# Kernel optimization log

Hardware: AMD Instinct MI355X
Metric: run time of the kernel (lower is better)

Reference implementation:

```python
import jax, jax.numpy as jnp
import numpy as np

N_ENT = 50000
N_REL = 500
N_DIM = 256
K = 4            # num_blocks; n_arity = 3 -> arch has K**3 = 64 entries
B = 1024


def setup_inputs() -> dict:
    key = jax.random.key(0)
    k0, k1, k2, k3 = jax.random.split(key, 4)
    facts = jax.random.randint(k0, (B, 3), 0, N_REL)          # head, tail, rela (all < n_rel <= n_ent)
    arch = jax.random.randint(k1, (K ** 3,), 0, 3)            # selects op in {0, 1, -1}
    ent_w = jax.random.normal(k2, (N_ENT, N_DIM), dtype=jnp.float32) * 0.05  # xavier-ish scale
    rel_w = jax.random.normal(k3, (N_REL, N_DIM), dtype=jnp.float32) * 0.05
    return {
        "facts": facts,
        "arch": arch,
        "ent_w": ent_w,
        "rel_w": rel_w,
        "bne_gamma": jnp.ones((N_DIM,), jnp.float32),
        "bne_beta": jnp.zeros((N_DIM,), jnp.float32),
        "bnr_gamma": jnp.ones((N_DIM,), jnp.float32),
        "bnr_beta": jnp.zeros((N_DIM,), jnp.float32),
    }


def _bn(x, gamma, beta, eps=1e-5):
    # BatchNorm1d in training mode: biased batch statistics over the batch dim.
    m = jnp.mean(x, axis=0)
    v = jnp.var(x, axis=0)
    return (x - m) * jax.lax.rsqrt(v + eps) * gamma + beta


def _bce(p, y):
    # torch F.binary_cross_entropy clamps log terms at -100
    logp = jnp.maximum(jnp.log(p), -100.0)
    log1mp = jnp.maximum(jnp.log1p(-p), -100.0)
    return -jnp.mean(y * logp + (1.0 - y) * log1mp)


def reference(facts, arch, ent_w, rel_w, bne_gamma, bne_beta, bnr_gamma, bnr_beta):
    L = N_DIM // K
    h, t, r = facts[:, 0], facts[:, 1], facts[:, 2]
    # separate BN calls for head / tail batches, as in the torch code (dropout is eval-mode identity)
    he = _bn(ent_w[h], bne_gamma, bne_beta).reshape(-1, K, L)   # [B, K, L]
    te = _bn(ent_w[t], bne_gamma, bne_beta).reshape(-1, K, L)
    re = _bn(rel_w[r], bnr_gamma, bnr_beta).reshape(-1, K, L)
    # alpha[i,j,k] = ops[op_idx[i*K*K + j*K + k]] in {0, 1, -1}
    alpha = jnp.asarray([0.0, 1.0, -1.0], dtype=ent_w.dtype)[arch].reshape(K, K, K)
    # fused extend + inner_vec + inner_alpha_bi + sum-over-blocks:
    # last_idx=2 (head side, rela x tail): vec[b,k,l] = sum_{i,j} alpha[i,j,k] r[b,i,l] t[b,j,l]
    head_vec = jnp.einsum('ijk,bil,bjl->bkl', alpha, re, te).reshape(-1, N_DIM)
    # last_idx=1 (tail side, rela x head): vec[b,k,l] = sum_{i,j} alpha[i,k,j] r[b,i,l] h[b,j,l]
    tail_vec = jnp.einsum('ikj,bil,bjl->bkl', alpha, re, he).reshape(-1, N_DIM)
    head_p = jax.nn.softmax(head_vec @ ent_w.T, axis=1)         # [B, N_ENT]
    tail_p = jax.nn.softmax(tail_vec @ ent_w.T, axis=1)
    head_label = jax.nn.one_hot(h, N_ENT, dtype=head_p.dtype)
    tail_label = jax.nn.one_hot(t, N_ENT, dtype=tail_p.dtype)
    return _bce(head_p, head_label) + _bce(tail_p, tail_label)
```

## Files before the change

### kernel.cpp

```cpp
#include <hip/hip_runtime.h>

#define N_ENT   50000
#define N_ENT_P 50048
#define NDIM    256
#define BATCH   1024
#define MROWS   2048
#define BM      128
#define BN      128
#define BK      64
#define NTILES  391
#define NSTRIP  32
#define SHIFT   30.0f

typedef __attribute__((ext_vector_type(8))) short short8;
typedef __attribute__((ext_vector_type(4))) float f32x4;

__device__ __forceinline__ unsigned short f2bf(float f) {
  unsigned int u = __float_as_uint(f);
  u += 0x7fffu + ((u >> 16) & 1u);
  return (unsigned short)(u >> 16);
}

__device__ __forceinline__ void async16(const void* g, void* lds) {
  __builtin_amdgcn_global_load_lds(
      (const __attribute__((address_space(1))) unsigned int*)g,
      (__attribute__((address_space(3))) unsigned int*)lds,
      16, 0, 0);
}

__global__ void k_convert(const float* __restrict__ ent_w,
                          unsigned short* __restrict__ Wb) {
  int t = blockIdx.x * 256 + threadIdx.x;
  int row = t >> 6, c4 = (t & 63) << 2;
  ushort4 v;
  if (row < N_ENT) {
    float4 f = *(const float4*)(ent_w + row * NDIM + c4);
    v.x = f2bf(f.x); v.y = f2bf(f.y); v.z = f2bf(f.z); v.w = f2bf(f.w);
  } else {
    v.x = v.y = v.z = v.w = 0;
  }
  *(ushort4*)(Wb + row * NDIM + c4) = v;
}

__global__ void k_stats(const int* __restrict__ facts,
                        const float* __restrict__ ent_w,
                        const float* __restrict__ rel_w,
                        float* __restrict__ stats) {
  int seg = blockIdx.y;
  int d = threadIdx.x;
  const float* tab = (seg == 2) ? rel_w : ent_w;
  int r0 = blockIdx.x * 16;
  int idxs[16];
#pragma unroll
  for (int i = 0; i < 16; ++i) idxs[i] = facts[(r0 + i) * 3 + seg];
  float s = 0.f, s2 = 0.f;
#pragma unroll
  for (int i = 0; i < 16; ++i) {
    float v = tab[idxs[i] * NDIM + d];
    s += v; s2 += v * v;
  }
  atomicAdd(&stats[(seg * 2 + 0) * NDIM + d], s);
  atomicAdd(&stats[(seg * 2 + 1) * NDIM + d], s2);
}

__global__ void k_vectors(const int* __restrict__ facts, const int* __restrict__ arch,
                          const float* __restrict__ ent_w, const float* __restrict__ rel_w,
                          const float* __restrict__ bne_g, const float* __restrict__ bne_b,
                          const float* __restrict__ bnr_g, const float* __restrict__ bnr_b,
                          const float* __restrict__ stats,
                          unsigned short* __restrict__ HVb, float* __restrict__ zlab) {
  __shared__ float sh_he[256], sh_te[256], sh_re[256], sh_alpha[64], sh_red[16];
  int b = blockIdx.x, d = threadIdx.x;
  int h = facts[b * 3 + 0], t = facts[b * 3 + 1], r = facts[b * 3 + 2];
  const float inv = 1.0f / (float)BATCH;
  float mh = stats[0 * 256 + d] * inv, vh = stats[1 * 256 + d] * inv - mh * mh;
  float mt = stats[2 * 256 + d] * inv, vt = stats[3 * 256 + d] * inv - mt * mt;
  float mr = stats[4 * 256 + d] * inv, vr = stats[5 * 256 + d] * inv - mr * mr;
  float sch = rsqrtf(vh + 1e-5f) * bne_g[d], shh = bne_b[d] - mh * sch;
  float sct = rsqrtf(vt + 1e-5f) * bne_g[d], sht = bne_b[d] - mt * sct;
  float scr = rsqrtf(vr + 1e-5f) * bnr_g[d], shr = bnr_b[d] - mr * scr;
  sh_he[d] = ent_w[h * NDIM + d] * sch + shh;
  sh_te[d] = ent_w[t * NDIM + d] * sct + sht;
  sh_re[d] = rel_w[r * NDIM + d] * scr + shr;
  if (d < 64) {
    int a = arch[d];
    sh_alpha[d] = (a == 0) ? 0.f : ((a == 1) ? 1.f : -1.f);
  }
  __syncthreads();
  int k = d >> 6, l = d & 63;
  float hv = 0.f, tv = 0.f;
#pragma unroll
  for (int i = 0; i < 4; ++i) {
    float re_i = sh_re[i * 64 + l];
#pragma unroll
    for (int j = 0; j < 4; ++j) {
      hv += sh_alpha[i * 16 + j * 4 + k] * re_i * sh_te[j * 64 + l];
      tv += sh_alpha[i * 16 + k * 4 + j] * re_i * sh_he[j * 64 + l];
    }
  }
  HVb[b * NDIM + d] = f2bf(hv);
  HVb[(BATCH + b) * NDIM + d] = f2bf(tv);
  float ph = hv * ent_w[h * NDIM + d];
  float pt = tv * ent_w[t * NDIM + d];
  for (int m = 1; m < 64; m <<= 1) { ph += __shfl_xor(ph, m); pt += __shfl_xor(pt, m); }
  int wid = d >> 6;
  if ((d & 63) == 0) { sh_red[wid] = ph; sh_red[8 + wid] = pt; }
  __syncthreads();
  if (d == 0) {
    zlab[b] = sh_red[0] + sh_red[1] + sh_red[2] + sh_red[3];
    zlab[BATCH + b] = sh_red[8] + sh_red[9] + sh_red[10] + sh_red[11];
  }
}

__global__ void __launch_bounds__(256, 2)
k_gemm(const unsigned short* __restrict__ HVb, const unsigned short* __restrict__ Wb,
       float* __restrict__ m1, float* __restrict__ m2) {
  __shared__ __align__(16) unsigned short As[BM * BK];
  __shared__ __align__(16) unsigned short Bs[BN * BK];
  const int tid = threadIdx.x;
  const int lane = tid & 63, wid = tid >> 6;
  const int L = blockIdx.x;
  const int xcd = L & 7, r = L >> 3;
  const int strip = xcd * 4 + (r >> 4);
  const int bm = (r & 15) * BM;
  const int wm = (wid & 1) * 64, wn = (wid >> 1) * 64;
  const int q = lane >> 4, ln = lane & 15;

  float ps1[4][4] = {}, ps2[4][4] = {};

  for (int nt = strip; nt < NTILES; nt += NSTRIP) {
    const int bn = nt * BN;
    f32x4 acc[4][4] = {};
    for (int kc = 0; kc < NDIM; kc += BK) {
      __syncthreads();
#pragma unroll
      for (int c = 0; c < 4; ++c) {
        int G = (wid * 4 + c) * 64 + lane;
        int row = G >> 3, slot = G & 7;
        int kg = slot ^ (row & 7);
        async16(HVb + (bm + row) * NDIM + kc + kg * 8,
                (char*)As + (wid * 4 + c) * 1024);
        async16(Wb + (bn + row) * NDIM + kc + kg * 8,
                (char*)Bs + (wid * 4 + c) * 1024);
      }
      __syncthreads();
#pragma unroll
      for (int kk = 0; kk < BK; kk += 32) {
        short8 a[4], bb[4];
        int kg = (kk >> 3) + q;
#pragma unroll
        for (int mi = 0; mi < 4; ++mi) {
          int row = wm + mi * 16 + ln;
          a[mi] = *(const short8*)((const char*)As + row * 128 + ((kg ^ (row & 7)) << 4));
        }
#pragma unroll
        for (int ni = 0; ni < 4; ++ni) {
          int row = wn + ni * 16 + ln;
          bb[ni] = *(const short8*)((const char*)Bs + row * 128 + ((kg ^ (row & 7)) << 4));
        }
#pragma unroll
        for (int mi = 0; mi < 4; ++mi)
#pragma unroll
          for (int ni = 0; ni < 4; ++ni)
            acc[mi][ni] = __builtin_amdgcn_mfma_f32_16x16x32_bf16(a[mi], bb[ni], acc[mi][ni], 0, 0, 0);
      }
    }
#pragma unroll
    for (int mi = 0; mi < 4; ++mi)
#pragma unroll
      for (int reg = 0; reg < 4; ++reg) {
        float s1 = 0.f, s2 = 0.f;
#pragma unroll
        for (int ni = 0; ni < 4; ++ni) {
          float e1 = __expf(acc[mi][ni][reg] - SHIFT);
          s1 += e1; s2 += e1 * e1;
        }
        ps1[mi][reg] += s1;
        ps2[mi][reg] += s2;
      }
  }

#pragma unroll
  for (int mi = 0; mi < 4; ++mi)
#pragma unroll
    for (int reg = 0; reg < 4; ++reg) {
      float s1 = ps1[mi][reg], s2 = ps2[mi][reg];
      for (int m = 1; m < 16; m <<= 1) { s1 += __shfl_xor(s1, m); s2 += __shfl_xor(s2, m); }
      if (ln == 0) {
        int grow = bm + wm + mi * 16 + q * 4 + reg;
        atomicAdd(&m1[grow], s1);
        atomicAdd(&m2[grow], s2);
      }
    }
}

__global__ void k_finalize(const float* __restrict__ m1, const float* __restrict__ m2,
                           const float* __restrict__ zlab, float* __restrict__ out) {
  __shared__ float red[16];
  int tid = threadIdx.x;
  float local = 0.f;
  for (int r = tid; r < MROWS; r += 1024) {
    float M1 = m1[r];
    float lse = SHIFT + logf(M1);
    float zl = zlab[r];
    float lp = fmaxf(zl - lse, -100.f);
    float pl = __expf(zl - lse);
    float l1m = fmaxf(log1pf(-pl), -100.f);
    float iM1 = 1.f / M1;
    float r2 = m2[r] * iM1 * iM1;
    float series = -(1.f + 0.5f * r2);
    local += lp - l1m + series;
  }
  for (int m = 1; m < 64; m <<= 1) local += __shfl_xor(local, m);
  if ((tid & 63) == 0) red[tid >> 6] = local;
  __syncthreads();
  if (tid == 0) {
    float s = 0.f;
    for (int i = 0; i < 16; ++i) s += red[i];
    out[0] = -s / ((float)BATCH * (float)N_ENT);
  }
}

extern "C" void kernel_launch(void* const* d_in, const int* in_sizes, int n_in,
                              void* d_out, int out_size, void* d_ws, size_t ws_size,
                              hipStream_t stream) {
  const int* facts = (const int*)d_in[0];
  const int* arch = (const int*)d_in[1];
  const float* ent_w = (const float*)d_in[2];
  const float* rel_w = (const float*)d_in[3];
  const float* bne_g = (const float*)d_in[4];
  const float* bne_b = (const float*)d_in[5];
  const float* bnr_g = (const float*)d_in[6];
  const float* bnr_b = (const float*)d_in[7];
  char* ws = (char*)d_ws;
  float* stats = (float*)ws;
  float* m1 = (float*)(ws + 6144);
  float* m2 = (float*)(ws + 14336);
  float* zlab = (float*)(ws + 22528);
  unsigned short* HVb = (unsigned short*)(ws + 30720);
  unsigned short* Wb = (unsigned short*)(ws + 30720 + 1048576);

  hipMemsetAsync(ws, 0, 22528, stream);
  k_convert<<<dim3((N_ENT_P * 64) / 256), dim3(256), 0, stream>>>(ent_w, Wb);
  k_stats<<<dim3(64, 3), dim3(256), 0, stream>>>(facts, ent_w, rel_w, stats);
  k_vectors<<<dim3(BATCH), dim3(256), 0, stream>>>(facts, arch, ent_w, rel_w,
                                                   bne_g, bne_b, bnr_g, bnr_b,
                                                   stats, HVb, zlab);
  k_gemm<<<dim3(512), dim3(256), 0, stream>>>(HVb, Wb, m1, m2);
  k_finalize<<<dim3(1), dim3(1024), 0, stream>>>(m1, m2, zlab, (float*)d_out);
}
```

Before: 174.7 us.

## Pipeline GEMM B tiles through a 4-stage LDS ring with resident A tile

The GEMM now loads each block's full 128x256 A tile into LDS once and streams 256-wide B tiles in 32-wide K chunks through a 4-deep async buffer ring. Each chunk step uses a single barrier guarded by a partial vmcnt wait, replacing the old load-sync-compute cycle with two barriers per step. Blocks grow to 512 threads with BN=256, the grid halves, and the entity padding grows to a multiple of 256. LDS use rises to about 128KB per block, so only one block fits per CU, and the larger padding adds wasted columns that the finalize step must account for.

```diff
diff --git a/kernel.cpp b/kernel.cpp
--- a/kernel.cpp
+++ b/kernel.cpp
@@ -1,15 +1,14 @@
 #include <hip/hip_runtime.h>
 
 #define N_ENT   50000
-#define N_ENT_P 50048
+#define N_ENT_P 50176
 #define NDIM    256
 #define BATCH   1024
 #define MROWS   2048
 #define BM      128
-#define BN      128
-#define BK      64
-#define NTILES  391
-#define NSTRIP  32
+#define BN      256
+#define NTILES  196
+#define NSTRIP  16
 #define SHIFT   30.0f
 
 typedef __attribute__((ext_vector_type(8))) short short8;
@@ -112,58 +111,79 @@
   }
 }
 
-__global__ void __launch_bounds__(256, 2)
+__global__ void __launch_bounds__(512, 2)
 k_gemm(const unsigned short* __restrict__ HVb, const unsigned short* __restrict__ Wb,
        float* __restrict__ m1, float* __restrict__ m2) {
-  __shared__ __align__(16) unsigned short As[BM * BK];
-  __shared__ __align__(16) unsigned short Bs[BN * BK];
+  __shared__ __align__(16) unsigned short As[4 * BM * 64];
+  __shared__ __align__(16) unsigned short Bs[4 * BN * 32];
   const int tid = threadIdx.x;
   const int lane = tid & 63, wid = tid >> 6;
   const int L = blockIdx.x;
-  const int xcd = L & 7, r = L >> 3;
-  const int strip = xcd * 4 + (r >> 4);
-  const int bm = (r & 15) * BM;
-  const int wm = (wid & 1) * 64, wn = (wid >> 1) * 64;
+  const int xcd = L & 7, rr = L >> 3;
+  const int strip = xcd * 2 + (rr >> 4);
+  const int bm = (rr & 15) * BM;
+  const int wm = (wid >> 2) * 64, wn = (wid & 3) * 64;
   const int q = lane >> 4, ln = lane & 15;
 
+  const int ntmine = NTILES / NSTRIP + (strip < (NTILES % NSTRIP) ? 1 : 0);
+  const int njobs = ntmine * 8;
+
+#pragma unroll
+  for (int c = 0; c < 4; ++c)
+#pragma unroll
+    for (int i = 0; i < 2; ++i) {
+      int G = (wid * 2 + i) * 64 + lane;
+      int row = G >> 3, slot = G & 7;
+      int kg = slot ^ (row & 7);
+      async16(HVb + (bm + row) * NDIM + c * 64 + kg * 8,
+              (char*)As + c * 16384 + (wid * 2 + i) * 1024);
+    }
+
+  auto stageB = [&](int j2) {
+    int jj = (j2 < njobs) ? j2 : 0;
+    int nt = strip + (jj >> 3) * NSTRIP;
+    int kc = (jj & 7) * 32;
+    int buf = j2 & 3;
+#pragma unroll
+    for (int i = 0; i < 2; ++i) {
+      int G = (wid * 2 + i) * 64 + lane;
+      int row = G >> 2, slot = G & 3;
+      int kg = slot ^ ((row >> 1) & 3);
+      async16(Wb + (nt * BN + row) * NDIM + kc + kg * 8,
+              (char*)Bs + buf * 16384 + (wid * 2 + i) * 1024);
+    }
+  };
+  stageB(0); stageB(1); stageB(2);
+
   float ps1[4][4] = {}, ps2[4][4] = {};
-
-  for (int nt = strip; nt < NTILES; nt += NSTRIP) {
-    const int bn = nt * BN;
+  int j = 0;
+  for (int ti = 0; ti < ntmine; ++ti) {
     f32x4 acc[4][4] = {};
-    for (int kc = 0; kc < NDIM; kc += BK) {
-      __syncthreads();
-#pragma unroll
-      for (int c = 0; c < 4; ++c) {
-        int G = (wid * 4 + c) * 64 + lane;
-        int row = G >> 3, slot = G & 7;
-        int kg = slot ^ (row & 7);
-        async16(HVb + (bm + row) * NDIM + kc + kg * 8,
-                (char*)As + (wid * 4 + c) * 1024);
-        async16(Wb + (bn + row) * NDIM + kc + kg * 8,
-                (char*)Bs + (wid * 4 + c) * 1024);
-      }
-      __syncthreads();
-#pragma unroll
-      for (int kk = 0; kk < BK; kk += 32) {
-        short8 a[4], bb[4];
-        int kg = (kk >> 3) + q;
-#pragma unroll
-        for (int mi = 0; mi < 4; ++mi) {
-          int row = wm + mi * 16 + ln;
-          a[mi] = *(const short8*)((const char*)As + row * 128 + ((kg ^ (row & 7)) << 4));
-        }
-#pragma unroll
-        for (int ni = 0; ni < 4; ++ni) {
-          int row = wn + ni * 16 + ln;
-          bb[ni] = *(const short8*)((const char*)Bs + row * 128 + ((kg ^ (row & 7)) << 4));
-        }
-#pragma unroll
-        for (int mi = 0; mi < 4; ++mi)
-#pragma unroll
-          for (int ni = 0; ni < 4; ++ni)
-            acc[mi][ni] = __builtin_amdgcn_mfma_f32_16x16x32_bf16(a[mi], bb[ni], acc[mi][ni], 0, 0, 0);
-      }
+#pragma unroll
+    for (int c = 0; c < 8; ++c, ++j) {
+      asm volatile("s_waitcnt vmcnt(4)" ::: "memory");
+      __builtin_amdgcn_s_barrier();
+      asm volatile("" ::: "memory");
+      stageB(j + 3);
+      const char* Ac = (const char*)As + (c >> 1) * 16384;
+      const char* Bc = (const char*)Bs + (c & 3) * 16384;
+      const int kga = ((c & 1) << 2) + q;
+      short8 a[4], bb[4];
+#pragma unroll
+      for (int mi = 0; mi < 4; ++mi) {
+        int row = wm + mi * 16 + ln;
+        a[mi] = *(const short8*)(Ac + row * 128 + ((kga ^ (row & 7)) << 4));
+      }
+#pragma unroll
+      for (int ni = 0; ni < 4; ++ni) {
+        int row = wn + ni * 16 + ln;
+        bb[ni] = *(const short8*)(Bc + row * 64 + ((q ^ ((row >> 1) & 3)) << 4));
+      }
+#pragma unroll
+      for (int mi = 0; mi < 4; ++mi)
+#pragma unroll
+        for (int ni = 0; ni < 4; ++ni)
+          acc[mi][ni] = __builtin_amdgcn_mfma_f32_16x16x32_bf16(a[mi], bb[ni], acc[mi][ni], 0, 0, 0);
     }
 #pragma unroll
     for (int mi = 0; mi < 4; ++mi)
@@ -179,6 +199,7 @@
         ps2[mi][reg] += s2;
       }
   }
+  asm volatile("s_waitcnt vmcnt(0)" ::: "memory");
 
 #pragma unroll
   for (int mi = 0; mi < 4; ++mi)
@@ -246,6 +267,6 @@
   k_vectors<<<dim3(BATCH), dim3(256), 0, stream>>>(facts, arch, ent_w, rel_w,
                                                    bne_g, bne_b, bnr_g, bnr_b,
                                                    stats, HVb, zlab);
-  k_gemm<<<dim3(512), dim3(256), 0, stream>>>(HVb, Wb, m1, m2);
+  k_gemm<<<dim3(256), dim3(512), 0, stream>>>(HVb, Wb, m1, m2);
   k_finalize<<<dim3(1), dim3(1024), 0, stream>>>(m1, m2, zlab, (float*)d_out);
 }
```

Result: no change. 176.6 us (+1.1%).

## Pre-swizzle entity weights into MFMA fragment layout and stream B from global

Applied to the files above, without the earlier changes.

The bf16 conversion kernel now writes entity weights directly in the per-lane MFMA fragment order, in 16-row tiles. The GEMM keeps the whole 64-row A block resident in LDS, loaded once. It reads B fragments straight from global memory with coalesced short8 loads, double-buffered in registers, so the per-k-chunk LDS staging and barriers are gone. Tiles become 64x256 with each wave owning 64 columns, and s_setprio is raised around MFMA bursts. The cost is global-load latency exposed on the B path, plus a few more padded rows.

```diff
diff --git a/kernel.cpp b/kernel.cpp
--- a/kernel.cpp
+++ b/kernel.cpp
@@ -1,15 +1,14 @@
 #include <hip/hip_runtime.h>
 
 #define N_ENT   50000
-#define N_ENT_P 50048
+#define N_ENT_P 50176
 #define NDIM    256
 #define BATCH   1024
 #define MROWS   2048
-#define BM      128
-#define BN      128
-#define BK      64
-#define NTILES  391
-#define NSTRIP  32
+#define AM      64
+#define BN      256
+#define NTILES  196
+#define NSTRIP  16
 #define SHIFT   30.0f
 
 typedef __attribute__((ext_vector_type(8))) short short8;
@@ -30,16 +29,27 @@
 
 __global__ void k_convert(const float* __restrict__ ent_w,
                           unsigned short* __restrict__ Wb) {
-  int t = blockIdx.x * 256 + threadIdx.x;
-  int row = t >> 6, c4 = (t & 63) << 2;
-  ushort4 v;
-  if (row < N_ENT) {
-    float4 f = *(const float4*)(ent_w + row * NDIM + c4);
-    v.x = f2bf(f.x); v.y = f2bf(f.y); v.z = f2bf(f.z); v.w = f2bf(f.w);
-  } else {
-    v.x = v.y = v.z = v.w = 0;
-  }
-  *(ushort4*)(Wb + row * NDIM + c4) = v;
+  int nt = blockIdx.x;
+  int tid = threadIdx.x;
+#pragma unroll
+  for (int h = 0; h < 2; ++h) {
+    int g = h * 256 + tid;
+    int kc = g >> 6, lane = g & 63;
+    int qq = lane >> 4, lnn = lane & 15;
+    int row = nt * 16 + lnn, col = kc * 32 + qq * 8;
+    short8 v;
+    if (row < N_ENT) {
+      const float* s = ent_w + row * NDIM + col;
+      float4 f0 = *(const float4*)s, f1 = *(const float4*)(s + 4);
+      v[0] = (short)f2bf(f0.x); v[1] = (short)f2bf(f0.y);
+      v[2] = (short)f2bf(f0.z); v[3] = (short)f2bf(f0.w);
+      v[4] = (short)f2bf(f1.x); v[5] = (short)f2bf(f1.y);
+      v[6] = (short)f2bf(f1.z); v[7] = (short)f2bf(f1.w);
+    } else {
+      v = (short8)(0);
+    }
+    *(short8*)(Wb + nt * 4096 + g * 8) = v;
+  }
 }
 
 __global__ void k_stats(const int* __restrict__ facts,
@@ -115,56 +125,77 @@
 __global__ void __launch_bounds__(256, 2)
 k_gemm(const unsigned short* __restrict__ HVb, const unsigned short* __restrict__ Wb,
        float* __restrict__ m1, float* __restrict__ m2) {
-  __shared__ __align__(16) unsigned short As[BM * BK];
-  __shared__ __align__(16) unsigned short Bs[BN * BK];
+  __shared__ __align__(16) unsigned short As[4 * AM * 64];
   const int tid = threadIdx.x;
-  const int lane = tid & 63, wid = tid >> 6;
+  const int lane = tid & 63, wn4 = tid >> 6;
   const int L = blockIdx.x;
-  const int xcd = L & 7, r = L >> 3;
-  const int strip = xcd * 4 + (r >> 4);
-  const int bm = (r & 15) * BM;
-  const int wm = (wid & 1) * 64, wn = (wid >> 1) * 64;
+  const int xcd = L & 7, rr = L >> 3;
+  const int strip = xcd * 2 + (rr >> 5);
+  const int bm = (rr & 31) * AM;
   const int q = lane >> 4, ln = lane & 15;
 
+  const int ntmine = NTILES / NSTRIP + (strip < (NTILES % NSTRIP) ? 1 : 0);
+
+#pragma unroll
+  for (int c = 0; c < 4; ++c)
+#pragma unroll
+    for (int i = 0; i < 2; ++i) {
+      int G = i * 256 + tid;
+      int row = G >> 3, slot = G & 7;
+      int kg = slot ^ (row & 7);
+      async16(HVb + (bm + row) * NDIM + c * 64 + kg * 8,
+              (char*)As + c * 8192 + G * 16);
+    }
+
+  int aoffq[4];
+#pragma unroll
+  for (int mi = 0; mi < 4; ++mi) {
+    int row = mi * 16 + ln;
+    aoffq[mi] = row * 128 + ((q ^ (row & 7)) << 4);
+  }
+
+  __syncthreads();
+
+  const unsigned short* bp =
+      Wb + (size_t)strip * 65536 + (size_t)wn4 * 16384 + (size_t)lane * 8;
+
+  short8 fa0[4], fa1[4], fb0[4], fb1[4];
   float ps1[4][4] = {}, ps2[4][4] = {};
 
-  for (int nt = strip; nt < NTILES; nt += NSTRIP) {
-    const int bn = nt * BN;
+#define RDA(CN, FA)                                                           \
+  {                                                                           \
+    const char* Ac = (const char*)As + ((((CN)) & 7) >> 1) * 8192;            \
+    const int axor = (((CN)) & 1) << 6;                                       \
+    _Pragma("unroll") for (int mi = 0; mi < 4; ++mi)                          \
+        FA[mi] = *(const short8*)(Ac + (aoffq[mi] ^ axor));                   \
+  }
+#define RDB(BP, CN, FB)                                                       \
+  _Pragma("unroll") for (int ni = 0; ni < 4; ++ni)                            \
+      FB[ni] = *(const short8*)((BP) + (CN) * 512 + ni * 4096);
+#define MM(FA, FB)                                                            \
+  {                                                                           \
+    __builtin_amdgcn_s_setprio(1);                                            \
+    _Pragma("unroll") for (int mi = 0; mi < 4; ++mi)                          \
+        _Pragma("unroll") for (int ni = 0; ni < 4; ++ni)                      \
+            acc[mi][ni] = __builtin_amdgcn_mfma_f32_16x16x32_bf16(            \
+                FA[mi], FB[ni], acc[mi][ni], 0, 0, 0);                        \
+    __builtin_amdgcn_s_setprio(0);                                            \
+  }
+
+  RDA(0, fa0); RDB(bp, 0, fb0);
+  for (int ti = 0; ti < ntmine; ++ti) {
+    const unsigned short* bpn =
+        (ti + 1 < ntmine) ? bp + (size_t)NSTRIP * 65536 : bp;
     f32x4 acc[4][4] = {};
-    for (int kc = 0; kc < NDIM; kc += BK) {
-      __syncthreads();
-#pragma unroll
-      for (int c = 0; c < 4; ++c) {
-        int G = (wid * 4 + c) * 64 + lane;
-        int row = G >> 3, slot = G & 7;
-        int kg = slot ^ (row & 7);
-        async16(HVb + (bm + row) * NDIM + kc + kg * 8,
-                (char*)As + (wid * 4 + c) * 1024);
-        async16(Wb + (bn + row) * NDIM + kc + kg * 8,
-                (char*)Bs + (wid * 4 + c) * 1024);
-      }
-      __syncthreads();
-#pragma unroll
-      for (int kk = 0; kk < BK; kk += 32) {
-        short8 a[4], bb[4];
-        int kg = (kk >> 3) + q;
-#pragma unroll
-        for (int mi = 0; mi < 4; ++mi) {
-          int row = wm + mi * 16 + ln;
-          a[mi] = *(const short8*)((const char*)As + row * 128 + ((kg ^ (row & 7)) << 4));
-        }
-#pragma unroll
-        for (int ni = 0; ni < 4; ++ni) {
-          int row = wn + ni * 16 + ln;
-          bb[ni] = *(const short8*)((const char*)Bs + row * 128 + ((kg ^ (row & 7)) << 4));
-        }
-#pragma unroll
-        for (int mi = 0; mi < 4; ++mi)
-#pragma unroll
-          for (int ni = 0; ni < 4; ++ni)
-            acc[mi][ni] = __builtin_amdgcn_mfma_f32_16x16x32_bf16(a[mi], bb[ni], acc[mi][ni], 0, 0, 0);
-      }
-    }
+    RDA(1, fa1); RDB(bp, 1, fb1);  MM(fa0, fb0);
+    RDA(2, fa0); RDB(bp, 2, fb0);  MM(fa1, fb1);
+    RDA(3, fa1); RDB(bp, 3, fb1);  MM(fa0, fb0);
+    RDA(4, fa0); RDB(bp, 4, fb0);  MM(fa1, fb1);
+    RDA(5, fa1); RDB(bp, 5, fb1);  MM(fa0, fb0);
+    RDA(6, fa0); RDB(bp, 6, fb0);  MM(fa1, fb1);
+    RDA(7, fa1); RDB(bp, 7, fb1);  MM(fa0, fb0);
+    RDA(0, fa0); RDB(bpn, 0, fb0); MM(fa1, fb1);
+    bp = bpn;
 #pragma unroll
     for (int mi = 0; mi < 4; ++mi)
 #pragma unroll
@@ -179,6 +210,9 @@
         ps2[mi][reg] += s2;
       }
   }
+#undef MM
+#undef RDB
+#undef RDA
 
 #pragma unroll
   for (int mi = 0; mi < 4; ++mi)
@@ -187,7 +221,7 @@
       float s1 = ps1[mi][reg], s2 = ps2[mi][reg];
       for (int m = 1; m < 16; m <<= 1) { s1 += __shfl_xor(s1, m); s2 += __shfl_xor(s2, m); }
       if (ln == 0) {
-        int grow = bm + wm + mi * 16 + q * 4 + reg;
+        int grow = bm + mi * 16 + q * 4 + reg;
         atomicAdd(&m1[grow], s1);
         atomicAdd(&m2[grow], s2);
       }
@@ -241,7 +275,7 @@
   unsigned short* Wb = (unsigned short*)(ws + 30720 + 1048576);
 
   hipMemsetAsync(ws, 0, 22528, stream);
-  k_convert<<<dim3((N_ENT_P * 64) / 256), dim3(256), 0, stream>>>(ent_w, Wb);
+  k_convert<<<dim3(N_ENT_P / 16), dim3(256), 0, stream>>>(ent_w, Wb);
   k_stats<<<dim3(64, 3), dim3(256), 0, stream>>>(facts, ent_w, rel_w, stats);
   k_vectors<<<dim3(BATCH), dim3(256), 0, stream>>>(facts, arch, ent_w, rel_w,
                                                    bne_g, bne_b, bnr_g, bnr_b,
```

After: 172.7 us. About the same (-1.1%).
